# Performance work log

Measured on AMD Instinct MI355X. Metric: run time of the kernel, lower is better.

## Reference

```python
import jax, jax.numpy as jnp
import numpy as np
import math

B, T, D = 2, 1024, 128
H, DH = 64, 2
SCALE = math.sqrt(DH)
TEMPERATURE = 0.8

def setup_inputs() -> dict:
    key = jax.random.key(0)
    ks = jax.random.split(key, 5)
    inv = 1.0 / math.sqrt(D)
    return {
        "x": jax.random.normal(ks[0], (B, T, D), dtype=jnp.float32),
        "Wq": jax.random.normal(ks[1], (D, D), dtype=jnp.float32) * inv,
        "Wk": jax.random.normal(ks[2], (D, D), dtype=jnp.float32) * inv,
        "Wv": jax.random.normal(ks[3], (D, D), dtype=jnp.float32) * inv,
        "Wo": jax.random.normal(ks[4], (D, D), dtype=jnp.float32) * inv,
    }

def reference(x, Wq, Wk, Wv, Wo):
    b, t, d = x.shape
    # torch nn.Linear(bias=False): y = x @ W.T
    Q = (x @ Wq.T).reshape(b, t, H, DH).transpose(0, 2, 1, 3)  # (B,H,T,dh)
    K = (x @ Wk.T).reshape(b, t, H, DH).transpose(0, 2, 1, 3)
    V = (x @ Wv.T).reshape(b, t, H, DH).transpose(0, 2, 1, 3)
    # scores / sqrt(d_head) / temperature, causal mask (strict upper -> -inf)
    scores = jnp.einsum("bhqd,bhkd->bhqk", Q, K) / (SCALE * TEMPERATURE)
    causal = jnp.triu(jnp.ones((t, t), dtype=bool), k=1)  # True above diagonal
    scores = jnp.where(causal, -jnp.inf, scores)
    attn = jax.nn.softmax(scores, axis=-1)  # dropout is identity in eval mode
    out = jnp.einsum("bhqk,bhkd->bhqd", attn, V)
    out = out.transpose(0, 2, 1, 3).reshape(b, t, d)
    return out @ Wo.T
```

## Files before the change

kernel.cpp:

```cpp
#include <hip/hip_runtime.h>
#include <math.h>

#define Tdim 1024
#define Hh   64

__device__ __constant__ float kQScale = 0.8838834764831844f * 1.4426950408889634f;

__global__ __launch_bounds__(256) void qkv_proj(
    const float* __restrict__ x, const float* __restrict__ Wq,
    const float* __restrict__ Wk, const float* __restrict__ Wv,
    float* __restrict__ Q, float* __restrict__ KV)
{
    __shared__ float xs[16][128];
    __shared__ float Wch[128][36];

    const int tid  = threadIdx.x;
    const int row0 = blockIdx.x * 16;
    const int w    = blockIdx.y;

    {
        const float4* xg = reinterpret_cast<const float4*>(x + (size_t)row0 * 128);
        reinterpret_cast<float4*>(&xs[0][0])[tid]       = xg[tid];
        reinterpret_cast<float4*>(&xs[0][0])[tid + 256] = xg[tid + 256];
    }

    const float* W = (w == 0) ? Wq : (w == 1) ? Wk : Wv;

    const int j0 = tid & 31;
    const int r0 = (tid >> 5) << 1;

    float acc[2][4];
#pragma unroll
    for (int r = 0; r < 2; ++r)
#pragma unroll
        for (int c = 0; c < 4; ++c) acc[r][c] = 0.f;

    for (int ch = 0; ch < 4; ++ch) {
        __syncthreads();
#pragma unroll
        for (int s = 0; s < 4; ++s) {
            const int idx  = tid + s * 256;
            const int rowW = idx >> 3;
            const int c4   = idx & 7;
            *reinterpret_cast<float4*>(&Wch[rowW][c4 * 4]) =
                reinterpret_cast<const float4*>(W + (size_t)rowW * 128 + ch * 32)[c4];
        }
        __syncthreads();

#pragma unroll
        for (int c = 0; c < 8; ++c) {
            const float4 w0 = *reinterpret_cast<const float4*>(&Wch[j0      ][c * 4]);
            const float4 w1 = *reinterpret_cast<const float4*>(&Wch[j0 + 32 ][c * 4]);
            const float4 w2 = *reinterpret_cast<const float4*>(&Wch[j0 + 64 ][c * 4]);
            const float4 w3 = *reinterpret_cast<const float4*>(&Wch[j0 + 96 ][c * 4]);
#pragma unroll
            for (int r = 0; r < 2; ++r) {
                const float4 xv = *reinterpret_cast<const float4*>(&xs[r0 + r][ch * 32 + c * 4]);
                acc[r][0] = fmaf(xv.x, w0.x, fmaf(xv.y, w0.y, fmaf(xv.z, w0.z, fmaf(xv.w, w0.w, acc[r][0]))));
                acc[r][1] = fmaf(xv.x, w1.x, fmaf(xv.y, w1.y, fmaf(xv.z, w1.z, fmaf(xv.w, w1.w, acc[r][1]))));
                acc[r][2] = fmaf(xv.x, w2.x, fmaf(xv.y, w2.y, fmaf(xv.z, w2.z, fmaf(xv.w, w2.w, acc[r][2]))));
                acc[r][3] = fmaf(xv.x, w3.x, fmaf(xv.y, w3.y, fmaf(xv.z, w3.z, fmaf(xv.w, w3.w, acc[r][3]))));
            }
        }
    }

#pragma unroll
    for (int r = 0; r < 2; ++r) {
        const int row = row0 + r0 + r;
        const int bb  = row >> 10;
        const int t   = row & 1023;
#pragma unroll
        for (int jj = 0; jj < 4; ++jj) {
            const int j = j0 + jj * 32;
            const float v = acc[r][jj];
            if (w == 0) {
                Q[(size_t)row * 128 + j] = v * kQScale;
            } else {
                const int h  = j >> 1, dh = j & 1;
                const int bh = bb * Hh + h;
                KV[((size_t)bh * Tdim + t) * 4 + ((w == 1) ? dh : 2 + dh)] = v;
            }
        }
    }
}

__global__ __launch_bounds__(256) void attn(
    const float* __restrict__ Q, const float4* __restrict__ KV,
    float* __restrict__ O)
{
    __shared__ float4 KVs[Tdim];
    const int tid   = threadIdx.x;
    const int chunk = blockIdx.x;
    const int bh    = blockIdx.y;
    const int nk    = chunk * 64 + 64;

    const float4* KVg = KV + (size_t)bh * Tdim;
    for (int i = tid; i < nk; i += 256) KVs[i] = KVg[i];
    __syncthreads();

    const int t   = chunk * 64 + (tid >> 2);
    const int sub = tid & 3;
    const int b   = bh >> 6, h = bh & 63;
    const float2 q = *reinterpret_cast<const float2*>(
        Q + (size_t)(b * Tdim + t) * 128 + h * 2);

    float l = 0.f, a0 = 0.f, a1 = 0.f;
#pragma unroll 4
    for (int k = sub; k <= t; k += 4) {
        const float4 kv = KVs[k];
        const float p = exp2f(fmaf(q.x, kv.x, q.y * kv.y));
        l  += p;
        a0 = fmaf(p, kv.z, a0);
        a1 = fmaf(p, kv.w, a1);
    }

    l  += __shfl_xor(l, 1);  l  += __shfl_xor(l, 2);
    a0 += __shfl_xor(a0, 1); a0 += __shfl_xor(a0, 2);
    a1 += __shfl_xor(a1, 1); a1 += __shfl_xor(a1, 2);

    if (sub == 0) {
        const float rl = 1.0f / l;
        float* Op = O + (size_t)(b * Tdim + t) * 128 + h * 2;
        Op[0] = a0 * rl;
        Op[1] = a1 * rl;
    }
}

__global__ __launch_bounds__(256) void out_proj(
    const float* __restrict__ Oin, const float* __restrict__ Wo,
    float* __restrict__ out)
{
    __shared__ float xs[16][128];
    __shared__ float Wch[128][36];

    const int tid  = threadIdx.x;
    const int row0 = blockIdx.x * 16;

    {
        const float4* xg = reinterpret_cast<const float4*>(Oin + (size_t)row0 * 128);
        reinterpret_cast<float4*>(&xs[0][0])[tid]       = xg[tid];
        reinterpret_cast<float4*>(&xs[0][0])[tid + 256] = xg[tid + 256];
    }

    const int j0 = tid & 31;
    const int r0 = (tid >> 5) << 1;

    float acc[2][4];
#pragma unroll
    for (int r = 0; r < 2; ++r)
#pragma unroll
        for (int c = 0; c < 4; ++c) acc[r][c] = 0.f;

    for (int ch = 0; ch < 4; ++ch) {
        __syncthreads();
#pragma unroll
        for (int s = 0; s < 4; ++s) {
            const int idx  = tid + s * 256;
            const int rowW = idx >> 3;
            const int c4   = idx & 7;
            *reinterpret_cast<float4*>(&Wch[rowW][c4 * 4]) =
                reinterpret_cast<const float4*>(Wo + (size_t)rowW * 128 + ch * 32)[c4];
        }
        __syncthreads();

#pragma unroll
        for (int c = 0; c < 8; ++c) {
            const float4 w0 = *reinterpret_cast<const float4*>(&Wch[j0      ][c * 4]);
            const float4 w1 = *reinterpret_cast<const float4*>(&Wch[j0 + 32 ][c * 4]);
            const float4 w2 = *reinterpret_cast<const float4*>(&Wch[j0 + 64 ][c * 4]);
            const float4 w3 = *reinterpret_cast<const float4*>(&Wch[j0 + 96 ][c * 4]);
#pragma unroll
            for (int r = 0; r < 2; ++r) {
                const float4 xv = *reinterpret_cast<const float4*>(&xs[r0 + r][ch * 32 + c * 4]);
                acc[r][0] = fmaf(xv.x, w0.x, fmaf(xv.y, w0.y, fmaf(xv.z, w0.z, fmaf(xv.w, w0.w, acc[r][0]))));
                acc[r][1] = fmaf(xv.x, w1.x, fmaf(xv.y, w1.y, fmaf(xv.z, w1.z, fmaf(xv.w, w1.w, acc[r][1]))));
                acc[r][2] = fmaf(xv.x, w2.x, fmaf(xv.y, w2.y, fmaf(xv.z, w2.z, fmaf(xv.w, w2.w, acc[r][2]))));
                acc[r][3] = fmaf(xv.x, w3.x, fmaf(xv.y, w3.y, fmaf(xv.z, w3.z, fmaf(xv.w, w3.w, acc[r][3]))));
            }
        }
    }

#pragma unroll
    for (int r = 0; r < 2; ++r) {
        const int row = row0 + r0 + r;
#pragma unroll
        for (int jj = 0; jj < 4; ++jj) {
            const int j = j0 + jj * 32;
            out[(size_t)row * 128 + j] = acc[r][jj];
        }
    }
}

extern "C" void kernel_launch(void* const* d_in, const int* in_sizes, int n_in,
                              void* d_out, int out_size, void* d_ws, size_t ws_size,
                              hipStream_t stream) {
    const float* x  = (const float*)d_in[0];
    const float* Wq = (const float*)d_in[1];
    const float* Wk = (const float*)d_in[2];
    const float* Wv = (const float*)d_in[3];
    const float* Wo = (const float*)d_in[4];
    float* out = (float*)d_out;

    float* ws = (float*)d_ws;
    float* Q  = ws;
    float* KV = ws + 262144;
    float* O  = ws + 786432;

    qkv_proj<<<dim3(128, 3), 256, 0, stream>>>(x, Wq, Wk, Wv, Q, KV);
    attn<<<dim3(16, 128), 256, 0, stream>>>(Q, (const float4*)KV, O);
    out_proj<<<128, 256, 0, stream>>>(O, Wo, out);
}
```

Baseline: 117.3 us.

## Rewrite projections as register-resident rows and block attention over four queries

Both projection kernels now use one 64-thread wavefront per block. Each lane holds a full input row of x in registers and reads weight rows straight from global memory as wave-uniform broadcasts, replacing the shared-memory weight tiling. Results are staged through a small LDS tile so the Q and output writes are coalesced float4 stores. The attention kernel gives each 8-lane group four consecutive queries so every K/V load from LDS is reused four times, and it launches chunks in reverse order so the longest causal chunks start first. The new projection layout uses many registers and launches small blocks, which may limit occupancy or latency hiding.

```diff
diff --git a/kernel.cpp b/kernel.cpp
--- a/kernel.cpp
+++ b/kernel.cpp
@@ -6,80 +6,63 @@
 
 __device__ __constant__ float kQScale = 0.8838834764831844f * 1.4426950408889634f;
 
-__global__ __launch_bounds__(256) void qkv_proj(
+__global__ __launch_bounds__(64) void qkv_proj(
     const float* __restrict__ x, const float* __restrict__ Wq,
     const float* __restrict__ Wk, const float* __restrict__ Wv,
     float* __restrict__ Q, float* __restrict__ KV)
 {
-    __shared__ float xs[16][128];
-    __shared__ float Wch[128][36];
-
-    const int tid  = threadIdx.x;
-    const int row0 = blockIdx.x * 16;
-    const int w    = blockIdx.y;
-
+    __shared__ __align__(16) float Ot[64][20];
+
+    const int lane = threadIdx.x;
+    const int row  = blockIdx.x * 64 + lane;
+    const int jb   = blockIdx.y * 16;
+    const int mat  = blockIdx.z;
+    const float* W = (mat == 0) ? Wq : (mat == 1) ? Wk : Wv;
+
+    float4 xr[32];
     {
-        const float4* xg = reinterpret_cast<const float4*>(x + (size_t)row0 * 128);
-        reinterpret_cast<float4*>(&xs[0][0])[tid]       = xg[tid];
-        reinterpret_cast<float4*>(&xs[0][0])[tid + 256] = xg[tid + 256];
-    }
-
-    const float* W = (w == 0) ? Wq : (w == 1) ? Wk : Wv;
-
-    const int j0 = tid & 31;
-    const int r0 = (tid >> 5) << 1;
-
-    float acc[2][4];
-#pragma unroll
-    for (int r = 0; r < 2; ++r)
-#pragma unroll
-        for (int c = 0; c < 4; ++c) acc[r][c] = 0.f;
-
-    for (int ch = 0; ch < 4; ++ch) {
+        const float4* xrow = reinterpret_cast<const float4*>(x + (size_t)row * 128);
+#pragma unroll
+        for (int k = 0; k < 32; ++k) xr[k] = xrow[k];
+    }
+
+    for (int cg = 0; cg < 4; ++cg) {
+        const float4* w0 = reinterpret_cast<const float4*>(W + (size_t)(jb + cg * 4 + 0) * 128);
+        const float4* w1 = reinterpret_cast<const float4*>(W + (size_t)(jb + cg * 4 + 1) * 128);
+        const float4* w2 = reinterpret_cast<const float4*>(W + (size_t)(jb + cg * 4 + 2) * 128);
+        const float4* w3 = reinterpret_cast<const float4*>(W + (size_t)(jb + cg * 4 + 3) * 128);
+        float a0 = 0.f, a1 = 0.f, a2 = 0.f, a3 = 0.f;
+#pragma unroll
+        for (int k = 0; k < 32; ++k) {
+            const float4 xv = xr[k];
+            const float4 v0 = w0[k], v1 = w1[k], v2 = w2[k], v3 = w3[k];
+            a0 = fmaf(xv.x, v0.x, fmaf(xv.y, v0.y, fmaf(xv.z, v0.z, fmaf(xv.w, v0.w, a0))));
+            a1 = fmaf(xv.x, v1.x, fmaf(xv.y, v1.y, fmaf(xv.z, v1.z, fmaf(xv.w, v1.w, a1))));
+            a2 = fmaf(xv.x, v2.x, fmaf(xv.y, v2.y, fmaf(xv.z, v2.z, fmaf(xv.w, v2.w, a2))));
+            a3 = fmaf(xv.x, v3.x, fmaf(xv.y, v3.y, fmaf(xv.z, v3.z, fmaf(xv.w, v3.w, a3))));
+        }
+        if (mat == 0) {
+            Ot[lane][cg * 4 + 0] = a0 * kQScale;
+            Ot[lane][cg * 4 + 1] = a1 * kQScale;
+            Ot[lane][cg * 4 + 2] = a2 * kQScale;
+            Ot[lane][cg * 4 + 3] = a3 * kQScale;
+        } else {
+            const int tl = row & 1023, b = row >> 10;
+            const int h0 = (jb + cg * 4) >> 1;
+            const int off = (mat == 1) ? 0 : 2;
+            float* base = KV + (((size_t)(b * Hh + h0) * Tdim + tl) * 4 + off);
+            *reinterpret_cast<float2*>(base)        = make_float2(a0, a1);
+            *reinterpret_cast<float2*>(base + 4096) = make_float2(a2, a3);
+        }
+    }
+
+    if (mat == 0) {
         __syncthreads();
 #pragma unroll
-        for (int s = 0; s < 4; ++s) {
-            const int idx  = tid + s * 256;
-            const int rowW = idx >> 3;
-            const int c4   = idx & 7;
-            *reinterpret_cast<float4*>(&Wch[rowW][c4 * 4]) =
-                reinterpret_cast<const float4*>(W + (size_t)rowW * 128 + ch * 32)[c4];
-        }
-        __syncthreads();
-
-#pragma unroll
-        for (int c = 0; c < 8; ++c) {
-            const float4 w0 = *reinterpret_cast<const float4*>(&Wch[j0      ][c * 4]);
-            const float4 w1 = *reinterpret_cast<const float4*>(&Wch[j0 + 32 ][c * 4]);
-            const float4 w2 = *reinterpret_cast<const float4*>(&Wch[j0 + 64 ][c * 4]);
-            const float4 w3 = *reinterpret_cast<const float4*>(&Wch[j0 + 96 ][c * 4]);
-#pragma unroll
-            for (int r = 0; r < 2; ++r) {
-                const float4 xv = *reinterpret_cast<const float4*>(&xs[r0 + r][ch * 32 + c * 4]);
-                acc[r][0] = fmaf(xv.x, w0.x, fmaf(xv.y, w0.y, fmaf(xv.z, w0.z, fmaf(xv.w, w0.w, acc[r][0]))));
-                acc[r][1] = fmaf(xv.x, w1.x, fmaf(xv.y, w1.y, fmaf(xv.z, w1.z, fmaf(xv.w, w1.w, acc[r][1]))));
-                acc[r][2] = fmaf(xv.x, w2.x, fmaf(xv.y, w2.y, fmaf(xv.z, w2.z, fmaf(xv.w, w2.w, acc[r][2]))));
-                acc[r][3] = fmaf(xv.x, w3.x, fmaf(xv.y, w3.y, fmaf(xv.z, w3.z, fmaf(xv.w, w3.w, acc[r][3]))));
-            }
-        }
-    }
-
-#pragma unroll
-    for (int r = 0; r < 2; ++r) {
-        const int row = row0 + r0 + r;
-        const int bb  = row >> 10;
-        const int t   = row & 1023;
-#pragma unroll
-        for (int jj = 0; jj < 4; ++jj) {
-            const int j = j0 + jj * 32;
-            const float v = acc[r][jj];
-            if (w == 0) {
-                Q[(size_t)row * 128 + j] = v * kQScale;
-            } else {
-                const int h  = j >> 1, dh = j & 1;
-                const int bh = bb * Hh + h;
-                KV[((size_t)bh * Tdim + t) * 4 + ((w == 1) ? dh : 2 + dh)] = v;
-            }
+        for (int rep = 0; rep < 4; ++rep) {
+            const int r = rep * 16 + (lane >> 2), c4 = lane & 3;
+            const float4 v = *reinterpret_cast<const float4*>(&Ot[r][c4 * 4]);
+            *reinterpret_cast<float4*>(Q + (size_t)(blockIdx.x * 64 + r) * 128 + jb + c4 * 4) = v;
         }
     }
 }
@@ -90,104 +73,117 @@
 {
     __shared__ float4 KVs[Tdim];
     const int tid   = threadIdx.x;
-    const int chunk = blockIdx.x;
+    const int chunk = 7 - blockIdx.x;
     const int bh    = blockIdx.y;
-    const int nk    = chunk * 64 + 64;
+    const int nk    = chunk * 128 + 128;
 
     const float4* KVg = KV + (size_t)bh * Tdim;
     for (int i = tid; i < nk; i += 256) KVs[i] = KVg[i];
     __syncthreads();
 
-    const int t   = chunk * 64 + (tid >> 2);
-    const int sub = tid & 3;
+    const int g   = tid >> 3;
+    const int sub = tid & 7;
+    const int q0  = chunk * 128 + g * 4;
     const int b   = bh >> 6, h = bh & 63;
-    const float2 q = *reinterpret_cast<const float2*>(
-        Q + (size_t)(b * Tdim + t) * 128 + h * 2);
-
-    float l = 0.f, a0 = 0.f, a1 = 0.f;
-#pragma unroll 4
-    for (int k = sub; k <= t; k += 4) {
+
+    float2 q[4];
+    {
+        const float* Qp = Q + (size_t)(b * Tdim + q0) * 128 + h * 2;
+#pragma unroll
+        for (int i = 0; i < 4; ++i)
+            q[i] = *reinterpret_cast<const float2*>(Qp + (size_t)i * 128);
+    }
+
+    float l[4]  = {0.f, 0.f, 0.f, 0.f};
+    float a0[4] = {0.f, 0.f, 0.f, 0.f};
+    float a1[4] = {0.f, 0.f, 0.f, 0.f};
+
+#pragma unroll 2
+    for (int k = sub; k < q0; k += 8) {
         const float4 kv = KVs[k];
-        const float p = exp2f(fmaf(q.x, kv.x, q.y * kv.y));
-        l  += p;
-        a0 = fmaf(p, kv.z, a0);
-        a1 = fmaf(p, kv.w, a1);
-    }
-
-    l  += __shfl_xor(l, 1);  l  += __shfl_xor(l, 2);
-    a0 += __shfl_xor(a0, 1); a0 += __shfl_xor(a0, 2);
-    a1 += __shfl_xor(a1, 1); a1 += __shfl_xor(a1, 2);
+#pragma unroll
+        for (int i = 0; i < 4; ++i) {
+            const float p = exp2f(fmaf(q[i].x, kv.x, q[i].y * kv.y));
+            l[i] += p;
+            a0[i] = fmaf(p, kv.z, a0[i]);
+            a1[i] = fmaf(p, kv.w, a1[i]);
+        }
+    }
+    if (sub < 4) {
+        const float4 kv = KVs[q0 + sub];
+#pragma unroll
+        for (int i = 0; i < 4; ++i) {
+            if (sub <= i) {
+                const float p = exp2f(fmaf(q[i].x, kv.x, q[i].y * kv.y));
+                l[i] += p;
+                a0[i] = fmaf(p, kv.z, a0[i]);
+                a1[i] = fmaf(p, kv.w, a1[i]);
+            }
+        }
+    }
+
+#pragma unroll
+    for (int i = 0; i < 4; ++i) {
+        l[i]  += __shfl_xor(l[i], 1);  l[i]  += __shfl_xor(l[i], 2);  l[i]  += __shfl_xor(l[i], 4);
+        a0[i] += __shfl_xor(a0[i], 1); a0[i] += __shfl_xor(a0[i], 2); a0[i] += __shfl_xor(a0[i], 4);
+        a1[i] += __shfl_xor(a1[i], 1); a1[i] += __shfl_xor(a1[i], 2); a1[i] += __shfl_xor(a1[i], 4);
+    }
 
     if (sub == 0) {
-        const float rl = 1.0f / l;
-        float* Op = O + (size_t)(b * Tdim + t) * 128 + h * 2;
-        Op[0] = a0 * rl;
-        Op[1] = a1 * rl;
-    }
-}
-
-__global__ __launch_bounds__(256) void out_proj(
+        float* Op = O + (size_t)(b * Tdim + q0) * 128 + h * 2;
+#pragma unroll
+        for (int i = 0; i < 4; ++i) {
+            const float rl = 1.0f / l[i];
+            *reinterpret_cast<float2*>(Op + (size_t)i * 128) =
+                make_float2(a0[i] * rl, a1[i] * rl);
+        }
+    }
+}
+
+__global__ __launch_bounds__(64) void out_proj(
     const float* __restrict__ Oin, const float* __restrict__ Wo,
     float* __restrict__ out)
 {
-    __shared__ float xs[16][128];
-    __shared__ float Wch[128][36];
-
-    const int tid  = threadIdx.x;
-    const int row0 = blockIdx.x * 16;
-
+    __shared__ __align__(16) float Ot[64][20];
+
+    const int lane = threadIdx.x;
+    const int row  = blockIdx.x * 64 + lane;
+    const int jb   = blockIdx.y * 16;
+
+    float4 xr[32];
     {
-        const float4* xg = reinterpret_cast<const float4*>(Oin + (size_t)row0 * 128);
-        reinterpret_cast<float4*>(&xs[0][0])[tid]       = xg[tid];
-        reinterpret_cast<float4*>(&xs[0][0])[tid + 256] = xg[tid + 256];
-    }
-
-    const int j0 = tid & 31;
-    const int r0 = (tid >> 5) << 1;
-
-    float acc[2][4];
-#pragma unroll
-    for (int r = 0; r < 2; ++r)
-#pragma unroll
-        for (int c = 0; c < 4; ++c) acc[r][c] = 0.f;
-
-    for (int ch = 0; ch < 4; ++ch) {
-        __syncthreads();
-#pragma unroll
-        for (int s = 0; s < 4; ++s) {
-            const int idx  = tid + s * 256;
-            const int rowW = idx >> 3;
-            const int c4   = idx & 7;
-            *reinterpret_cast<float4*>(&Wch[rowW][c4 * 4]) =
-                reinterpret_cast<const float4*>(Wo + (size_t)rowW * 128 + ch * 32)[c4];
-        }
-        __syncthreads();
-
-#pragma unroll
-        for (int c = 0; c < 8; ++c) {
-            const float4 w0 = *reinterpret_cast<const float4*>(&Wch[j0      ][c * 4]);
-            const float4 w1 = *reinterpret_cast<const float4*>(&Wch[j0 + 32 ][c * 4]);
-            const float4 w2 = *reinterpret_cast<const float4*>(&Wch[j0 + 64 ][c * 4]);
-            const float4 w3 = *reinterpret_cast<const float4*>(&Wch[j0 + 96 ][c * 4]);
-#pragma unroll
-            for (int r = 0; r < 2; ++r) {
-                const float4 xv = *reinterpret_cast<const float4*>(&xs[r0 + r][ch * 32 + c * 4]);
-                acc[r][0] = fmaf(xv.x, w0.x, fmaf(xv.y, w0.y, fmaf(xv.z, w0.z, fmaf(xv.w, w0.w, acc[r][0]))));
-                acc[r][1] = fmaf(xv.x, w1.x, fmaf(xv.y, w1.y, fmaf(xv.z, w1.z, fmaf(xv.w, w1.w, acc[r][1]))));
-                acc[r][2] = fmaf(xv.x, w2.x, fmaf(xv.y, w2.y, fmaf(xv.z, w2.z, fmaf(xv.w, w2.w, acc[r][2]))));
-                acc[r][3] = fmaf(xv.x, w3.x, fmaf(xv.y, w3.y, fmaf(xv.z, w3.z, fmaf(xv.w, w3.w, acc[r][3]))));
-            }
-        }
-    }
-
-#pragma unroll
-    for (int r = 0; r < 2; ++r) {
-        const int row = row0 + r0 + r;
-#pragma unroll
-        for (int jj = 0; jj < 4; ++jj) {
-            const int j = j0 + jj * 32;
-            out[(size_t)row * 128 + j] = acc[r][jj];
-        }
+        const float4* xrow = reinterpret_cast<const float4*>(Oin + (size_t)row * 128);
+#pragma unroll
+        for (int k = 0; k < 32; ++k) xr[k] = xrow[k];
+    }
+
+    for (int cg = 0; cg < 4; ++cg) {
+        const float4* w0 = reinterpret_cast<const float4*>(Wo + (size_t)(jb + cg * 4 + 0) * 128);
+        const float4* w1 = reinterpret_cast<const float4*>(Wo + (size_t)(jb + cg * 4 + 1) * 128);
+        const float4* w2 = reinterpret_cast<const float4*>(Wo + (size_t)(jb + cg * 4 + 2) * 128);
+        const float4* w3 = reinterpret_cast<const float4*>(Wo + (size_t)(jb + cg * 4 + 3) * 128);
+        float a0 = 0.f, a1 = 0.f, a2 = 0.f, a3 = 0.f;
+#pragma unroll
+        for (int k = 0; k < 32; ++k) {
+            const float4 xv = xr[k];
+            const float4 v0 = w0[k], v1 = w1[k], v2 = w2[k], v3 = w3[k];
+            a0 = fmaf(xv.x, v0.x, fmaf(xv.y, v0.y, fmaf(xv.z, v0.z, fmaf(xv.w, v0.w, a0))));
+            a1 = fmaf(xv.x, v1.x, fmaf(xv.y, v1.y, fmaf(xv.z, v1.z, fmaf(xv.w, v1.w, a1))));
+            a2 = fmaf(xv.x, v2.x, fmaf(xv.y, v2.y, fmaf(xv.z, v2.z, fmaf(xv.w, v2.w, a2))));
+            a3 = fmaf(xv.x, v3.x, fmaf(xv.y, v3.y, fmaf(xv.z, v3.z, fmaf(xv.w, v3.w, a3))));
+        }
+        Ot[lane][cg * 4 + 0] = a0;
+        Ot[lane][cg * 4 + 1] = a1;
+        Ot[lane][cg * 4 + 2] = a2;
+        Ot[lane][cg * 4 + 3] = a3;
+    }
+
+    __syncthreads();
+#pragma unroll
+    for (int rep = 0; rep < 4; ++rep) {
+        const int r = rep * 16 + (lane >> 2), c4 = lane & 3;
+        const float4 v = *reinterpret_cast<const float4*>(&Ot[r][c4 * 4]);
+        *reinterpret_cast<float4*>(out + (size_t)(blockIdx.x * 64 + r) * 128 + jb + c4 * 4) = v;
     }
 }
 
@@ -206,7 +202,7 @@
     float* KV = ws + 262144;
     float* O  = ws + 786432;
 
-    qkv_proj<<<dim3(128, 3), 256, 0, stream>>>(x, Wq, Wk, Wv, Q, KV);
-    attn<<<dim3(16, 128), 256, 0, stream>>>(Q, (const float4*)KV, O);
-    out_proj<<<128, 256, 0, stream>>>(O, Wo, out);
-}
+    qkv_proj<<<dim3(32, 8, 3), 64, 0, stream>>>(x, Wq, Wk, Wv, Q, KV);
+    attn<<<dim3(8, 128), 256, 0, stream>>>(Q, (const float4*)KV, O);
+    out_proj<<<dim3(32, 8), 64, 0, stream>>>(O, Wo, out);
+}
```

After: 156.7 us. 33.6% more time.
